# Performance work log

Measured on AMD Instinct MI355X. Metric: run time of the kernel, lower is better.

Reference implementation:

```python
import jax, jax.numpy as jnp
import numpy as np

N_NODES = 100000
N_EDGES = 1200000
NUM_GRAPHS = 128
IN_DIM = 5
HIDDEN = 64


def setup_inputs() -> dict:
    key = jax.random.key(0)
    ks = jax.random.split(key, 12)
    x = jax.random.normal(ks[0], (N_NODES, IN_DIM), dtype=jnp.float32)
    edge_index = jax.random.randint(ks[1], (2, N_EDGES), 0, N_NODES, dtype=jnp.int64 if jax.config.read('jax_enable_x64') else jnp.int32)
    batch = jnp.sort(jax.random.randint(ks[2], (N_NODES,), 0, NUM_GRAPHS, dtype=jnp.int32))
    s = lambda fan_in: 1.0 / np.sqrt(fan_in)
    return {
        'x': x,
        'edge_index': edge_index,
        'batch': batch,
        'w_rel1': jax.random.normal(ks[3], (IN_DIM, HIDDEN), dtype=jnp.float32) * s(IN_DIM),
        'b_rel1': jnp.zeros((HIDDEN,), dtype=jnp.float32),
        'w_root1': jax.random.normal(ks[4], (IN_DIM, HIDDEN), dtype=jnp.float32) * s(IN_DIM),
        'w_rel2': jax.random.normal(ks[5], (HIDDEN, HIDDEN), dtype=jnp.float32) * s(HIDDEN),
        'b_rel2': jnp.zeros((HIDDEN,), dtype=jnp.float32),
        'w_root2': jax.random.normal(ks[6], (HIDDEN, HIDDEN), dtype=jnp.float32) * s(HIDDEN),
        'w_h1': jax.random.normal(ks[7], (2 * HIDDEN, HIDDEN), dtype=jnp.float32) * s(2 * HIDDEN),
        'b_h1': jnp.zeros((HIDDEN,), dtype=jnp.float32),
        'w_h2': jax.random.normal(ks[8], (HIDDEN, 1), dtype=jnp.float32) * s(HIDDEN),
        'b_h2': jnp.zeros((1,), dtype=jnp.float32),
    }


def _graph_conv(x, src, dst, w_rel, b_rel, w_root):
    # PyG GraphConv (aggr='add'): out = aggr(x_src -> dst) @ W_rel + b_rel + x @ W_root
    agg = jax.ops.segment_sum(x[src], dst, num_segments=N_NODES)
    return agg @ w_rel + b_rel + x @ w_root


def reference(x, edge_index, batch,
              w_rel1, b_rel1, w_root1,
              w_rel2, b_rel2, w_root2,
              w_h1, b_h1, w_h2, b_h2):
    src, dst = edge_index[0], edge_index[1]
    h = jax.nn.relu(_graph_conv(x, src, dst, w_rel1, b_rel1, w_root1))
    h = jax.nn.relu(_graph_conv(h, src, dst, w_rel2, b_rel2, w_root2))
    # global add + mean pooling over graphs
    add_pool = jax.ops.segment_sum(h, batch, num_segments=NUM_GRAPHS)
    counts = jax.ops.segment_sum(jnp.ones((N_NODES,), h.dtype), batch, num_segments=NUM_GRAPHS)
    mean_pool = add_pool / jnp.maximum(counts, 1.0)[:, None]
    g = jnp.concatenate([mean_pool, add_pool], axis=1)  # [G, 2*HIDDEN]
    out = jax.nn.relu(g @ w_h1 + b_h1) @ w_h2 + b_h2
    return out.squeeze(-1)
```

## Files before the change

kernel.cpp:

```cpp
#include <hip/hip_runtime.h>
#include <hip/hip_bf16.h>

#define N_NODES    100000
#define N_EDGES    1200000
#define NUM_GRAPHS 128
#define IN_DIM     5
#define HIDDEN     64
#define M_TILES    (N_NODES / 16)
#define NI4        (N_EDGES / 4)

#define CB    391
#define CBLK  256
#define EPB   ((NI4 + CBLK - 1) / CBLK)

typedef __attribute__((ext_vector_type(8))) short short8;
typedef __attribute__((ext_vector_type(4))) float f32x4;

__device__ __forceinline__ unsigned short f2bs(float f) {
    union { float f; unsigned u; } v; v.f = f;
    return (unsigned short)((v.u + 0x7FFFu + ((v.u >> 16) & 1u)) >> 16);
}
__device__ __forceinline__ float bs2f(unsigned short s) {
    union { unsigned u; float f; } v; v.u = ((unsigned)s) << 16;
    return v.f;
}
__device__ __forceinline__ float blo(unsigned p) { return bs2f((unsigned short)(p & 0xffff)); }
__device__ __forceinline__ float bhi(unsigned p) { return bs2f((unsigned short)(p >> 16)); }
__device__ __forceinline__ unsigned pack2(float a, float b) {
    return ((unsigned)f2bs(b) << 16) | (unsigned)f2bs(a);
}

__device__ __forceinline__ unsigned char f2f8(float f) {
    union { float f; unsigned u; } v; v.f = f * 0x1p-120f;
    unsigned u = v.u + 0x7FFFFu + ((v.u >> 20) & 1u);
    return (unsigned char)(u >> 20);
}
__device__ __forceinline__ float f82f(unsigned b) {
    union { unsigned u; float f; } v; v.u = (b & 0x7Fu) << 20;
    return v.f * 0x1p120f;
}


__global__ void coarse_count(const int* __restrict__ dst, int* __restrict__ gcnt,
                             const float* __restrict__ x, uint4* __restrict__ xb) {
    __shared__ int h[CB];
    int t = threadIdx.x, b = blockIdx.x;
    for (int i = t; i < CB; i += 256) h[i] = 0;
    __syncthreads();
    int i0 = b * EPB, i1 = min(i0 + EPB, NI4);
    for (int i = i0 + t; i < i1; i += 256) {
        int4 d = ((const int4*)dst)[i];
        atomicAdd(&h[d.x >> 8], 1);
        atomicAdd(&h[d.y >> 8], 1);
        atomicAdd(&h[d.z >> 8], 1);
        atomicAdd(&h[d.w >> 8], 1);
    }
    __syncthreads();
    for (int i = t; i < CB; i += 256) gcnt[b * CB + i] = h[i];

    for (int n = b * 256 + t; n < N_NODES; n += CBLK * 256) {
        const float* xr = x + (size_t)n * IN_DIM;
        uint4 o;
        o.x = pack2(xr[0], xr[1]);
        o.y = pack2(xr[2], xr[3]);
        o.z = pack2(xr[4], 0.0f);
        o.w = 0u;
        xb[n] = o;
    }
}

__global__ void block_scan(int* __restrict__ gcnt, int* __restrict__ btot) {
    __shared__ int s[CBLK];
    int k = blockIdx.x, t = threadIdx.x;
    int v = gcnt[t * CB + k];
    s[t] = v;
    __syncthreads();
    for (int off = 1; off < CBLK; off <<= 1) {
        int u = (t >= off) ? s[t - off] : 0;
        __syncthreads();
        s[t] += u;
        __syncthreads();
    }
    gcnt[t * CB + k] = s[t] - v;
    if (t == CBLK - 1) btot[k] = s[t];
}

__global__ void bucket_scan(const int* __restrict__ btot, int* __restrict__ bstart,
                            float* __restrict__ add_pool, int* __restrict__ ptr) {
    __shared__ int s[512];
    int t = threadIdx.x;
    int v = (t < CB) ? btot[t] : 0;
    s[t] = v;
    __syncthreads();
    for (int off = 1; off < 512; off <<= 1) {
        int u = (t >= off) ? s[t - off] : 0;
        __syncthreads();
        s[t] += u;
        __syncthreads();
    }
    if (t < CB) bstart[t] = s[t] - v;
    if (t == 0) { bstart[CB] = N_EDGES; ptr[N_NODES] = N_EDGES; }
    for (int i = t; i < NUM_GRAPHS * HIDDEN; i += 512) add_pool[i] = 0.0f;
}

__global__ void partition_k(const int* __restrict__ src, const int* __restrict__ dst,
                            const int* __restrict__ gcnt, const int* __restrict__ bstart,
                            int* __restrict__ part) {
    __shared__ int base[CB];
    __shared__ int h[CB];
    int t = threadIdx.x, b = blockIdx.x;
    for (int i = t; i < CB; i += 256) {
        base[i] = bstart[i] + gcnt[b * CB + i];
        h[i] = 0;
    }
    __syncthreads();
    int i0 = b * EPB, i1 = min(i0 + EPB, NI4);
    for (int i = i0 + t; i < i1; i += 256) {
        int4 s4 = ((const int4*)src)[i];
        int4 d4 = ((const int4*)dst)[i];
        int k, r;
        k = d4.x >> 8; r = atomicAdd(&h[k], 1); part[base[k] + r] = s4.x | ((d4.x & 255) << 17);
        k = d4.y >> 8; r = atomicAdd(&h[k], 1); part[base[k] + r] = s4.y | ((d4.y & 255) << 17);
        k = d4.z >> 8; r = atomicAdd(&h[k], 1); part[base[k] + r] = s4.z | ((d4.z & 255) << 17);
        k = d4.w >> 8; r = atomicAdd(&h[k], 1); part[base[k] + r] = s4.w | ((d4.w & 255) << 17);
    }
}

__global__ void fine_gather1(const int* __restrict__ part, const int* __restrict__ bstart,
                             int* __restrict__ ptr, int* __restrict__ esrc,
                             const uint4* __restrict__ xb,
                             const float* __restrict__ x,
                             const float* __restrict__ w_rel1,
                             const float* __restrict__ b_rel1,
                             const float* __restrict__ w_root1,
                             unsigned short* __restrict__ h1,
                             unsigned char* __restrict__ h1f8) {
    __shared__ int fh[256];
    __shared__ int fo[256];
    __shared__ int fr[256];
    int k = blockIdx.x, t = threadIdx.x;
    int e0 = bstart[k], e1 = bstart[k + 1];
    fh[t] = 0; fr[t] = 0;
    __syncthreads();
    for (int e = e0 + t; e < e1; e += 256)
        atomicAdd(&fh[(part[e] >> 17) & 255], 1);
    __syncthreads();
    int v = fh[t];
    fo[t] = v;
    __syncthreads();
    for (int off = 1; off < 256; off <<= 1) {
        int u = (t >= off) ? fo[t - off] : 0;
        __syncthreads();
        fo[t] += u;
        __syncthreads();
    }
    int excl = fo[t] - v;
    int n_t = (k << 8) + t;
    if (n_t < N_NODES) ptr[n_t] = e0 + excl;
    fh[t] = excl;
    __syncthreads();
    for (int e = e0 + t; e < e1; e += 256) {
        int p = part[e];
        int d = (p >> 17) & 255;
        int r = atomicAdd(&fr[d], 1);
        esrc[e0 + fh[d] + r] = p & 0x1FFFF;
    }
    __syncthreads();

    int ql = t & 15;
    int g  = t >> 4;
    float wr[IN_DIM][4], wo[IN_DIM][4], bias[4];
#pragma unroll
    for (int j = 0; j < 4; ++j) {
        int ch = ql * 4 + j;
        bias[j] = b_rel1[ch];
#pragma unroll
        for (int kk = 0; kk < IN_DIM; ++kk) {
            wr[kk][j] = w_rel1[kk * HIDDEN + ch];
            wo[kk][j] = w_root1[kk * HIDDEN + ch];
        }
    }

    for (int nl = g; nl < 256; nl += 16) {
        int n = (k << 8) + nl;
        if (n >= N_NODES) break;
        int start = e0 + fh[nl];
        int end   = (nl < 255) ? (e0 + fh[nl + 1]) : e1;
        float a[IN_DIM] = {0.f, 0.f, 0.f, 0.f, 0.f};
        for (int e = start + ql; e < end; e += 16) {
            uint4 p = xb[esrc[e]];
            a[0] += blo(p.x); a[1] += bhi(p.x);
            a[2] += blo(p.y); a[3] += bhi(p.y);
            a[4] += blo(p.z);
        }
#pragma unroll
        for (int kk = 0; kk < IN_DIM; ++kk) {
            a[kk] += __shfl_xor(a[kk], 1, 64);
            a[kk] += __shfl_xor(a[kk], 2, 64);
            a[kk] += __shfl_xor(a[kk], 4, 64);
            a[kk] += __shfl_xor(a[kk], 8, 64);
        }
        float xr[IN_DIM];
#pragma unroll
        for (int kk = 0; kk < IN_DIM; ++kk) xr[kk] = x[(size_t)n * IN_DIM + kk];

        unsigned short hv[4];
        unsigned char  hf[4];
#pragma unroll
        for (int j = 0; j < 4; ++j) {
            float acc = bias[j];
#pragma unroll
            for (int kk = 0; kk < IN_DIM; ++kk)
                acc += a[kk] * wr[kk][j] + xr[kk] * wo[kk][j];
            float h = fmaxf(acc, 0.0f);
            hv[j] = f2bs(h);
            hf[j] = f2f8(h);
        }
        ushort4 v4; v4.x = hv[0]; v4.y = hv[1]; v4.z = hv[2]; v4.w = hv[3];
        *(ushort4*)(h1 + (size_t)n * HIDDEN + ql * 4) = v4;
        uchar4 c4; c4.x = hf[0]; c4.y = hf[1]; c4.z = hf[2]; c4.w = hf[3];
        *(uchar4*)(h1f8 + (size_t)n * HIDDEN + ql * 4) = c4;
    }
}


__global__ void gather2_fp8(const unsigned* __restrict__ rows,
                            const int* __restrict__ ptr,
                            const int* __restrict__ esrc,
                            uint2* __restrict__ agg2) {
    int t    = threadIdx.x;
    int ql   = t & 15;
    int grp  = (blockIdx.x * blockDim.x + t) >> 4;
    int ngrp = (gridDim.x * blockDim.x) >> 4;

    for (int n = grp; n < N_NODES; n += ngrp) {
        int start = ptr[n], end = ptr[n + 1];
        float4 a0 = {0.f,0.f,0.f,0.f}, a1 = a0, a2 = a0, a3 = a0;
        int e = start;
        for (; e + 3 < end; e += 4) {
            int s0 = esrc[e], s1 = esrc[e + 1], s2 = esrc[e + 2], s3 = esrc[e + 3];
            unsigned r0 = rows[(size_t)s0 * 16 + ql];
            unsigned r1 = rows[(size_t)s1 * 16 + ql];
            unsigned r2 = rows[(size_t)s2 * 16 + ql];
            unsigned r3 = rows[(size_t)s3 * 16 + ql];
            a0.x += f82f(r0); a0.y += f82f(r0 >> 8); a0.z += f82f(r0 >> 16); a0.w += f82f(r0 >> 24);
            a1.x += f82f(r1); a1.y += f82f(r1 >> 8); a1.z += f82f(r1 >> 16); a1.w += f82f(r1 >> 24);
            a2.x += f82f(r2); a2.y += f82f(r2 >> 8); a2.z += f82f(r2 >> 16); a2.w += f82f(r2 >> 24);
            a3.x += f82f(r3); a3.y += f82f(r3 >> 8); a3.z += f82f(r3 >> 16); a3.w += f82f(r3 >> 24);
        }
        for (; e < end; ++e) {
            unsigned r0 = rows[(size_t)esrc[e] * 16 + ql];
            a0.x += f82f(r0); a0.y += f82f(r0 >> 8); a0.z += f82f(r0 >> 16); a0.w += f82f(r0 >> 24);
        }
        float4 a;
        a.x = (a0.x + a1.x) + (a2.x + a3.x);
        a.y = (a0.y + a1.y) + (a2.y + a3.y);
        a.z = (a0.z + a1.z) + (a2.z + a3.z);
        a.w = (a0.w + a1.w) + (a2.w + a3.w);
        uint2 o;
        o.x = pack2(a.x, a.y);
        o.y = pack2(a.z, a.w);
        agg2[(size_t)n * 16 + ql] = o;
    }
}

__global__ void mlp2_pool(const unsigned short* __restrict__ agg2,
                          const unsigned short* __restrict__ h1,
                          const float* __restrict__ w_rel2,
                          const float* __restrict__ b_rel2,
                          const float* __restrict__ w_root2,
                          const int* __restrict__ batch,
                          float* __restrict__ add_pool) {
    int lane = threadIdx.x & 63;
    int wv   = threadIdx.x >> 6;
    int row  = lane & 15;
    int quad = lane >> 4;
    int n    = wv * 16 + row;

    short8 bwr[2], bwo[2];
#pragma unroll
    for (int s = 0; s < 2; ++s)
#pragma unroll
        for (int j = 0; j < 8; ++j) {
            int k = 32 * s + quad * 8 + j;
            bwr[s][j] = (short)f2bs(w_rel2[k * HIDDEN + n]);
            bwo[s][j] = (short)f2bs(w_root2[k * HIDDEN + n]);
        }
    float bias = b_rel2[n];

    for (int t = blockIdx.x; t < M_TILES; t += gridDim.x) {
        int m0 = t * 16;
        size_t rbase = (size_t)(m0 + row) * HIDDEN;
        short8 aa0 = *(const short8*)(agg2 + rbase + quad * 8);
        short8 aa1 = *(const short8*)(agg2 + rbase + 32 + quad * 8);
        short8 ah0 = *(const short8*)(h1   + rbase + quad * 8);
        short8 ah1 = *(const short8*)(h1   + rbase + 32 + quad * 8);

        f32x4 acc = {bias, bias, bias, bias};
        acc = __builtin_amdgcn_mfma_f32_16x16x32_bf16(aa0, bwr[0], acc, 0, 0, 0);
        acc = __builtin_amdgcn_mfma_f32_16x16x32_bf16(aa1, bwr[1], acc, 0, 0, 0);
        acc = __builtin_amdgcn_mfma_f32_16x16x32_bf16(ah0, bwo[0], acc, 0, 0, 0);
        acc = __builtin_amdgcn_mfma_f32_16x16x32_bf16(ah1, bwo[1], acc, 0, 0, 0);

        float hv0 = fmaxf(acc[0], 0.0f), hv1 = fmaxf(acc[1], 0.0f);
        float hv2 = fmaxf(acc[2], 0.0f), hv3 = fmaxf(acc[3], 0.0f);

        int gLo = batch[m0], gHi = batch[m0 + 15];
        if (gLo == gHi) {
            float s = (hv0 + hv1) + (hv2 + hv3);
            s += __shfl_xor(s, 16, 64);
            s += __shfl_xor(s, 32, 64);
            if (quad == 0)
                atomicAdd(&add_pool[gLo * HIDDEN + n], s);
        } else {
            int m = m0 + quad * 4;
            atomicAdd(&add_pool[batch[m]     * HIDDEN + n], hv0);
            atomicAdd(&add_pool[batch[m + 1] * HIDDEN + n], hv1);
            atomicAdd(&add_pool[batch[m + 2] * HIDDEN + n], hv2);
            atomicAdd(&add_pool[batch[m + 3] * HIDDEN + n], hv3);
        }
    }
}

__device__ __forceinline__ int lower_bound_i(const int* a, int n, int v) {
    int lo = 0, hi = n;
    while (lo < hi) { int mid = (lo + hi) >> 1; if (a[mid] < v) lo = mid + 1; else hi = mid; }
    return lo;
}

__global__ void head_mlp(const float* __restrict__ add_pool,
                         const int* __restrict__ batch,
                         const float* __restrict__ w_h1,
                         const float* __restrict__ b_h1,
                         const float* __restrict__ w_h2,
                         const float* __restrict__ b_h2,
                         float* __restrict__ out) {
    int g = blockIdx.x, t = threadIdx.x;

    __shared__ int s_cnt;
    if (t == 0) {
        int start = lower_bound_i(batch, N_NODES, g);
        int end   = lower_bound_i(batch, N_NODES, g + 1);
        s_cnt = end - start;
    }
    __syncthreads();
    float cnt = fmaxf((float)s_cnt, 1.0f);

    __shared__ float sg[2 * HIDDEN];
    float add = add_pool[(size_t)g * HIDDEN + t];
    sg[t]          = add / cnt;
    sg[HIDDEN + t] = add;
    __syncthreads();

    float hid = b_h1[t];
#pragma unroll 16
    for (int i = 0; i < 2 * HIDDEN; ++i)
        hid += sg[i] * w_h1[i * HIDDEN + t];
    hid = fmaxf(hid, 0.0f);

    float res = hid * w_h2[t];
    for (int off = 32; off > 0; off >>= 1)
        res += __shfl_down(res, off, 64);
    if (t == 0) out[g] = res + b_h2[0];
}

extern "C" void kernel_launch(void* const* d_in, const int* in_sizes, int n_in,
                              void* d_out, int out_size, void* d_ws, size_t ws_size,
                              hipStream_t stream) {
    const float* x       = (const float*)d_in[0];
    const int*   ei      = (const int*)d_in[1];
    const int*   src     = ei;
    const int*   dst     = ei + N_EDGES;
    const int*   batch   = (const int*)d_in[2];
    const float* w_rel1  = (const float*)d_in[3];
    const float* b_rel1  = (const float*)d_in[4];
    const float* w_root1 = (const float*)d_in[5];
    const float* w_rel2  = (const float*)d_in[6];
    const float* b_rel2  = (const float*)d_in[7];
    const float* w_root2 = (const float*)d_in[8];
    const float* w_h1    = (const float*)d_in[9];
    const float* b_h1    = (const float*)d_in[10];
    const float* w_h2    = (const float*)d_in[11];
    const float* b_h2    = (const float*)d_in[12];
    float* out = (float*)d_out;

    int* base = (int*)d_ws;
    int*   gcnt     = base;
    int*   btot     = gcnt + ((CBLK * CB + 3) & ~3);
    int*   bstart   = btot + ((CB + 3) & ~3);
    float* add_pool = (float*)(bstart + ((CB + 1 + 3) & ~3));
    int*   ptr      = (int*)(add_pool + NUM_GRAPHS * HIDDEN);
    int*   part     = ptr + ((N_NODES + 1 + 3) & ~3);
    int*   esrc     = part + N_EDGES;
    unsigned short* h1   = (unsigned short*)(esrc + N_EDGES);
    unsigned short* agg2 = h1 + (size_t)N_NODES * HIDDEN;
    unsigned char*  h1f8 = (unsigned char*)(agg2 + (size_t)N_NODES * HIDDEN);
    uint4*          xb   = (uint4*)(h1f8 + (size_t)N_NODES * HIDDEN);

    coarse_count<<<CBLK, 256, 0, stream>>>(dst, gcnt, x, xb);
    block_scan<<<CB, CBLK, 0, stream>>>(gcnt, btot);
    bucket_scan<<<1, 512, 0, stream>>>(btot, bstart, add_pool, ptr);
    partition_k<<<CBLK, 256, 0, stream>>>(src, dst, gcnt, bstart, part);

    fine_gather1<<<CB, 256, 0, stream>>>(part, bstart, ptr, esrc, xb, x,
                                         w_rel1, b_rel1, w_root1, h1, h1f8);
    gather2_fp8<<<2048, 256, 0, stream>>>((const unsigned*)h1f8, ptr, esrc, (uint2*)agg2);
    mlp2_pool<<<2048, 256, 0, stream>>>(agg2, h1, w_rel2, b_rel2, w_root2, batch, add_pool);
    head_mlp<<<NUM_GRAPHS, 64, 0, stream>>>(add_pool, batch, w_h1, b_h1, w_h2, b_h2, out);
}
```

Before: 195.4 us.

## Fuse CSR build kernels into one cooperative launch and use hardware fp8 conversion

The four preprocessing kernels (coarse count, per-bucket scan, bucket scan, partition) are merged into a single cooperative kernel that uses grid-wide syncs between phases. This removes three kernel launch gaps and their inter-kernel drain. The old four-launch path stays as a fallback if the cooperative launch fails. Separately, the fp8 gather decode now uses the packed hardware fp8-to-f32 conversion builtin when it is available, replacing manual bit manipulation. That conversion assumes the hardware fp8 format matches the custom encoding produced by f2f8, which looks like an E4M3-style bias trick and may not match exactly.

```diff
diff --git a/kernel.cpp b/kernel.cpp
--- a/kernel.cpp
+++ b/kernel.cpp
@@ -1,5 +1,8 @@
 #include <hip/hip_runtime.h>
 #include <hip/hip_bf16.h>
+#include <hip/hip_cooperative_groups.h>
+
+namespace cg = cooperative_groups;
 
 #define N_NODES    100000
 #define N_EDGES    1200000
@@ -15,6 +18,13 @@
 
 typedef __attribute__((ext_vector_type(8))) short short8;
 typedef __attribute__((ext_vector_type(4))) float f32x4;
+typedef __attribute__((ext_vector_type(2))) float f32x2;
+
+#if defined(__has_builtin)
+#if __has_builtin(__builtin_amdgcn_cvt_pk_f32_fp8)
+#define HAS_HWF8 1
+#endif
+#endif
 
 __device__ __forceinline__ unsigned short f2bs(float f) {
     union { float f; unsigned u; } v; v.f = f;
@@ -40,11 +50,28 @@
     return v.f * 0x1p120f;
 }
 
-
-__global__ void coarse_count(const int* __restrict__ dst, int* __restrict__ gcnt,
-                             const float* __restrict__ x, uint4* __restrict__ xb) {
+__device__ __forceinline__ void acc8(float4& a, unsigned r) {
+#ifdef HAS_HWF8
+    f32x2 lo = __builtin_amdgcn_cvt_pk_f32_fp8((int)r, false);
+    f32x2 hi = __builtin_amdgcn_cvt_pk_f32_fp8((int)r, true);
+    a.x += lo[0]; a.y += lo[1]; a.z += hi[0]; a.w += hi[1];
+#else
+    a.x += f82f(r); a.y += f82f(r >> 8); a.z += f82f(r >> 16); a.w += f82f(r >> 24);
+#endif
+}
+
+
+__global__ void coop_build(const int* __restrict__ src, const int* __restrict__ dst,
+                           int* __restrict__ gcnt, int* __restrict__ btot,
+                           int* __restrict__ bstart, int* __restrict__ part,
+                           int* __restrict__ ptr, float* __restrict__ add_pool,
+                           const float* __restrict__ x, uint4* __restrict__ xb) {
+    cg::grid_group grid = cg::this_grid();
     __shared__ int h[CB];
+    __shared__ int base[CB];
+    __shared__ int s[CBLK];
     int t = threadIdx.x, b = blockIdx.x;
+
     for (int i = t; i < CB; i += 256) h[i] = 0;
     __syncthreads();
     int i0 = b * EPB, i1 = min(i0 + EPB, NI4);
@@ -57,7 +84,98 @@
     }
     __syncthreads();
     for (int i = t; i < CB; i += 256) gcnt[b * CB + i] = h[i];
-
+    for (int n = b * 256 + t; n < N_NODES; n += CBLK * 256) {
+        const float* xr = x + (size_t)n * IN_DIM;
+        uint4 o;
+        o.x = pack2(xr[0], xr[1]);
+        o.y = pack2(xr[2], xr[3]);
+        o.z = pack2(xr[4], 0.0f);
+        o.w = 0u;
+        xb[n] = o;
+    }
+    __threadfence();
+    grid.sync();
+
+    for (int k = b; k < CB; k += CBLK) {
+        int v = gcnt[t * CB + k];
+        s[t] = v;
+        __syncthreads();
+        for (int off = 1; off < CBLK; off <<= 1) {
+            int u = (t >= off) ? s[t - off] : 0;
+            __syncthreads();
+            s[t] += u;
+            __syncthreads();
+        }
+        gcnt[t * CB + k] = s[t] - v;
+        if (t == CBLK - 1) btot[k] = s[t];
+        __syncthreads();
+    }
+    __threadfence();
+    grid.sync();
+
+    if (b == 0) {
+        if (t < 64) {
+            int cbase = t * 7;
+            int loc[7];
+            int sum = 0;
+#pragma unroll
+            for (int j = 0; j < 7; ++j) {
+                int idx = cbase + j;
+                int c = (idx < CB) ? btot[idx] : 0;
+                loc[j] = sum; sum += c;
+            }
+            int inc = sum;
+#pragma unroll
+            for (int off = 1; off < 64; off <<= 1) {
+                int u = __shfl_up(inc, off, 64);
+                if (t >= off) inc += u;
+            }
+            int excl = inc - sum;
+#pragma unroll
+            for (int j = 0; j < 7; ++j) {
+                int idx = cbase + j;
+                if (idx < CB) bstart[idx] = excl + loc[j];
+            }
+        }
+        if (t == 0) { bstart[CB] = N_EDGES; ptr[N_NODES] = N_EDGES; }
+    } else if (b == 1) {
+        for (int i = t; i < NUM_GRAPHS * HIDDEN; i += 256) add_pool[i] = 0.0f;
+    }
+    __threadfence();
+    grid.sync();
+
+    for (int i = t; i < CB; i += 256) {
+        base[i] = bstart[i] + gcnt[b * CB + i];
+        h[i] = 0;
+    }
+    __syncthreads();
+    for (int i = i0 + t; i < i1; i += 256) {
+        int4 s4 = ((const int4*)src)[i];
+        int4 d4 = ((const int4*)dst)[i];
+        int k, r;
+        k = d4.x >> 8; r = atomicAdd(&h[k], 1); part[base[k] + r] = s4.x | ((d4.x & 255) << 17);
+        k = d4.y >> 8; r = atomicAdd(&h[k], 1); part[base[k] + r] = s4.y | ((d4.y & 255) << 17);
+        k = d4.z >> 8; r = atomicAdd(&h[k], 1); part[base[k] + r] = s4.z | ((d4.z & 255) << 17);
+        k = d4.w >> 8; r = atomicAdd(&h[k], 1); part[base[k] + r] = s4.w | ((d4.w & 255) << 17);
+    }
+}
+
+__global__ void coarse_count(const int* __restrict__ dst, int* __restrict__ gcnt,
+                             const float* __restrict__ x, uint4* __restrict__ xb) {
+    __shared__ int h[CB];
+    int t = threadIdx.x, b = blockIdx.x;
+    for (int i = t; i < CB; i += 256) h[i] = 0;
+    __syncthreads();
+    int i0 = b * EPB, i1 = min(i0 + EPB, NI4);
+    for (int i = i0 + t; i < i1; i += 256) {
+        int4 d = ((const int4*)dst)[i];
+        atomicAdd(&h[d.x >> 8], 1);
+        atomicAdd(&h[d.y >> 8], 1);
+        atomicAdd(&h[d.z >> 8], 1);
+        atomicAdd(&h[d.w >> 8], 1);
+    }
+    __syncthreads();
+    for (int i = t; i < CB; i += 256) gcnt[b * CB + i] = h[i];
     for (int n = b * 256 + t; n < N_NODES; n += CBLK * 256) {
         const float* xr = x + (size_t)n * IN_DIM;
         uint4 o;
@@ -243,14 +361,11 @@
             unsigned r1 = rows[(size_t)s1 * 16 + ql];
             unsigned r2 = rows[(size_t)s2 * 16 + ql];
             unsigned r3 = rows[(size_t)s3 * 16 + ql];
-            a0.x += f82f(r0); a0.y += f82f(r0 >> 8); a0.z += f82f(r0 >> 16); a0.w += f82f(r0 >> 24);
-            a1.x += f82f(r1); a1.y += f82f(r1 >> 8); a1.z += f82f(r1 >> 16); a1.w += f82f(r1 >> 24);
-            a2.x += f82f(r2); a2.y += f82f(r2 >> 8); a2.z += f82f(r2 >> 16); a2.w += f82f(r2 >> 24);
-            a3.x += f82f(r3); a3.y += f82f(r3 >> 8); a3.z += f82f(r3 >> 16); a3.w += f82f(r3 >> 24);
+            acc8(a0, r0); acc8(a1, r1); acc8(a2, r2); acc8(a3, r3);
         }
         for (; e < end; ++e) {
             unsigned r0 = rows[(size_t)esrc[e] * 16 + ql];
-            a0.x += f82f(r0); a0.y += f82f(r0 >> 8); a0.z += f82f(r0 >> 16); a0.w += f82f(r0 >> 24);
+            acc8(a0, r0);
         }
         float4 a;
         a.x = (a0.x + a1.x) + (a2.x + a3.x);
@@ -397,10 +512,19 @@
     unsigned char*  h1f8 = (unsigned char*)(agg2 + (size_t)N_NODES * HIDDEN);
     uint4*          xb   = (uint4*)(h1f8 + (size_t)N_NODES * HIDDEN);
 
-    coarse_count<<<CBLK, 256, 0, stream>>>(dst, gcnt, x, xb);
-    block_scan<<<CB, CBLK, 0, stream>>>(gcnt, btot);
-    bucket_scan<<<1, 512, 0, stream>>>(btot, bstart, add_pool, ptr);
-    partition_k<<<CBLK, 256, 0, stream>>>(src, dst, gcnt, bstart, part);
+    {
+        void* ka[] = { (void*)&src, (void*)&dst, (void*)&gcnt, (void*)&btot,
+                       (void*)&bstart, (void*)&part, (void*)&ptr, (void*)&add_pool,
+                       (void*)&x, (void*)&xb };
+        hipError_t err = hipLaunchCooperativeKernel((const void*)coop_build,
+                                                    dim3(CBLK), dim3(256), ka, 0, stream);
+        if (err != hipSuccess) {
+            coarse_count<<<CBLK, 256, 0, stream>>>(dst, gcnt, x, xb);
+            block_scan<<<CB, CBLK, 0, stream>>>(gcnt, btot);
+            bucket_scan<<<1, 512, 0, stream>>>(btot, bstart, add_pool, ptr);
+            partition_k<<<CBLK, 256, 0, stream>>>(src, dst, gcnt, bstart, part);
+        }
+    }
 
     fine_gather1<<<CB, 256, 0, stream>>>(part, bstart, ptr, esrc, xb, x,
                                          w_rel1, b_rel1, w_root1, h1, h1f8);
```

Result: slower. 370.8 us (+89.8%).

## Fold scan kernels into partition, halve bucket width, use hardware fp8 convert

Applied to the files above, without the earlier changes.

The separate block_scan and bucket_scan launches are removed. Each partition_k block now computes its own prefix and the bucket totals by reading the whole gcnt column, followed by a wave-level scan, and add_pool zeroing moves into coarse_count. Buckets shrink from 256 to 128 nodes (782 buckets), which doubles fine_gather1 blocks and reduces per-block imbalance. The fp8 decode in gather2 uses the hardware packed conversion builtin when available. The cost is redundant per-block reads of gcnt (256×782 ints per block) and half-idle threads in the fine scan.

```diff
diff --git a/kernel.cpp b/kernel.cpp
--- a/kernel.cpp
+++ b/kernel.cpp
@@ -9,12 +9,19 @@
 #define M_TILES    (N_NODES / 16)
 #define NI4        (N_EDGES / 4)
 
-#define CB    391
+#define CB    782
 #define CBLK  256
 #define EPB   ((NI4 + CBLK - 1) / CBLK)
 
 typedef __attribute__((ext_vector_type(8))) short short8;
 typedef __attribute__((ext_vector_type(4))) float f32x4;
+typedef __attribute__((ext_vector_type(2))) float f32x2;
+
+#if defined(__has_builtin)
+#if __has_builtin(__builtin_amdgcn_cvt_pk_f32_fp8)
+#define HAS_HWF8 1
+#endif
+#endif
 
 __device__ __forceinline__ unsigned short f2bs(float f) {
     union { float f; unsigned u; } v; v.f = f;
@@ -40,9 +47,20 @@
     return v.f * 0x1p120f;
 }
 
+__device__ __forceinline__ void acc8(float4& a, unsigned r) {
+#ifdef HAS_HWF8
+    f32x2 lo = __builtin_amdgcn_cvt_pk_f32_fp8((int)r, false);
+    f32x2 hi = __builtin_amdgcn_cvt_pk_f32_fp8((int)r, true);
+    a.x += lo[0]; a.y += lo[1]; a.z += hi[0]; a.w += hi[1];
+#else
+    a.x += f82f(r); a.y += f82f(r >> 8); a.z += f82f(r >> 16); a.w += f82f(r >> 24);
+#endif
+}
+
 
 __global__ void coarse_count(const int* __restrict__ dst, int* __restrict__ gcnt,
-                             const float* __restrict__ x, uint4* __restrict__ xb) {
+                             const float* __restrict__ x, uint4* __restrict__ xb,
+                             float* __restrict__ add_pool, int* __restrict__ ptr) {
     __shared__ int h[CB];
     int t = threadIdx.x, b = blockIdx.x;
     for (int i = t; i < CB; i += 256) h[i] = 0;
@@ -50,10 +68,10 @@
     int i0 = b * EPB, i1 = min(i0 + EPB, NI4);
     for (int i = i0 + t; i < i1; i += 256) {
         int4 d = ((const int4*)dst)[i];
-        atomicAdd(&h[d.x >> 8], 1);
-        atomicAdd(&h[d.y >> 8], 1);
-        atomicAdd(&h[d.z >> 8], 1);
-        atomicAdd(&h[d.w >> 8], 1);
+        atomicAdd(&h[d.x >> 7], 1);
+        atomicAdd(&h[d.y >> 7], 1);
+        atomicAdd(&h[d.z >> 7], 1);
+        atomicAdd(&h[d.w >> 7], 1);
     }
     __syncthreads();
     for (int i = t; i < CB; i += 256) gcnt[b * CB + i] = h[i];
@@ -67,62 +85,75 @@
         o.w = 0u;
         xb[n] = o;
     }
-}
-
-__global__ void block_scan(int* __restrict__ gcnt, int* __restrict__ btot) {
-    __shared__ int s[CBLK];
-    int k = blockIdx.x, t = threadIdx.x;
-    int v = gcnt[t * CB + k];
-    s[t] = v;
-    __syncthreads();
-    for (int off = 1; off < CBLK; off <<= 1) {
-        int u = (t >= off) ? s[t - off] : 0;
-        __syncthreads();
-        s[t] += u;
-        __syncthreads();
-    }
-    gcnt[t * CB + k] = s[t] - v;
-    if (t == CBLK - 1) btot[k] = s[t];
-}
-
-__global__ void bucket_scan(const int* __restrict__ btot, int* __restrict__ bstart,
-                            float* __restrict__ add_pool, int* __restrict__ ptr) {
-    __shared__ int s[512];
-    int t = threadIdx.x;
-    int v = (t < CB) ? btot[t] : 0;
-    s[t] = v;
-    __syncthreads();
-    for (int off = 1; off < 512; off <<= 1) {
-        int u = (t >= off) ? s[t - off] : 0;
-        __syncthreads();
-        s[t] += u;
-        __syncthreads();
-    }
-    if (t < CB) bstart[t] = s[t] - v;
-    if (t == 0) { bstart[CB] = N_EDGES; ptr[N_NODES] = N_EDGES; }
-    for (int i = t; i < NUM_GRAPHS * HIDDEN; i += 512) add_pool[i] = 0.0f;
+    if (b == 0) {
+        for (int i = t; i < NUM_GRAPHS * HIDDEN; i += 256) add_pool[i] = 0.0f;
+        if (t == 0) ptr[N_NODES] = N_EDGES;
+    }
 }
 
 __global__ void partition_k(const int* __restrict__ src, const int* __restrict__ dst,
-                            const int* __restrict__ gcnt, const int* __restrict__ bstart,
+                            const int* __restrict__ gcnt, int* __restrict__ bstart,
                             int* __restrict__ part) {
-    __shared__ int base[CB];
+    __shared__ int sp[CB];
+    __shared__ int st[CB];
     __shared__ int h[CB];
     int t = threadIdx.x, b = blockIdx.x;
-    for (int i = t; i < CB; i += 256) {
-        base[i] = bstart[i] + gcnt[b * CB + i];
-        h[i] = 0;
-    }
-    __syncthreads();
+
+    for (int k = t; k < CB; k += 256) {
+        int pref = 0, tot = 0;
+        for (int bp = 0; bp < CBLK; ++bp) {
+            int v = gcnt[bp * CB + k];
+            tot += v;
+            if (bp < b) pref += v;
+        }
+        sp[k] = pref;
+        st[k] = tot;
+        h[k] = 0;
+    }
+    __syncthreads();
+
+    if (t < 64) {
+        int loc[13];
+        int base_i = t * 13;
+        int sum = 0;
+#pragma unroll
+        for (int j = 0; j < 13; ++j) {
+            int idx = base_i + j;
+            int c = (idx < CB) ? st[idx] : 0;
+            loc[j] = sum; sum += c;
+        }
+        int inc = sum;
+#pragma unroll
+        for (int off = 1; off < 64; off <<= 1) {
+            int u = __shfl_up(inc, off, 64);
+            if (t >= off) inc += u;
+        }
+        int excl = inc - sum;
+#pragma unroll
+        for (int j = 0; j < 13; ++j) {
+            int idx = base_i + j;
+            if (idx < CB) st[idx] = excl + loc[j];
+        }
+    }
+    __syncthreads();
+
+    for (int k = t; k < CB; k += 256) {
+        int bs = st[k];
+        sp[k] = bs + sp[k];
+        if (b == 0) bstart[k] = bs;
+    }
+    if (b == 0 && t == 0) bstart[CB] = N_EDGES;
+    __syncthreads();
+
     int i0 = b * EPB, i1 = min(i0 + EPB, NI4);
     for (int i = i0 + t; i < i1; i += 256) {
         int4 s4 = ((const int4*)src)[i];
         int4 d4 = ((const int4*)dst)[i];
         int k, r;
-        k = d4.x >> 8; r = atomicAdd(&h[k], 1); part[base[k] + r] = s4.x | ((d4.x & 255) << 17);
-        k = d4.y >> 8; r = atomicAdd(&h[k], 1); part[base[k] + r] = s4.y | ((d4.y & 255) << 17);
-        k = d4.z >> 8; r = atomicAdd(&h[k], 1); part[base[k] + r] = s4.z | ((d4.z & 255) << 17);
-        k = d4.w >> 8; r = atomicAdd(&h[k], 1); part[base[k] + r] = s4.w | ((d4.w & 255) << 17);
+        k = d4.x >> 7; r = atomicAdd(&h[k], 1); part[sp[k] + r] = s4.x | ((d4.x & 127) << 17);
+        k = d4.y >> 7; r = atomicAdd(&h[k], 1); part[sp[k] + r] = s4.y | ((d4.y & 127) << 17);
+        k = d4.z >> 7; r = atomicAdd(&h[k], 1); part[sp[k] + r] = s4.z | ((d4.z & 127) << 17);
+        k = d4.w >> 7; r = atomicAdd(&h[k], 1); part[sp[k] + r] = s4.w | ((d4.w & 127) << 17);
     }
 }
 
@@ -135,33 +166,35 @@
                              const float* __restrict__ w_root1,
                              unsigned short* __restrict__ h1,
                              unsigned char* __restrict__ h1f8) {
-    __shared__ int fh[256];
-    __shared__ int fo[256];
-    __shared__ int fr[256];
+    __shared__ int fh[128];
+    __shared__ int fo[128];
+    __shared__ int fr[128];
     int k = blockIdx.x, t = threadIdx.x;
     int e0 = bstart[k], e1 = bstart[k + 1];
-    fh[t] = 0; fr[t] = 0;
+    if (t < 128) { fh[t] = 0; fr[t] = 0; }
     __syncthreads();
     for (int e = e0 + t; e < e1; e += 256)
-        atomicAdd(&fh[(part[e] >> 17) & 255], 1);
-    __syncthreads();
-    int v = fh[t];
-    fo[t] = v;
-    __syncthreads();
-    for (int off = 1; off < 256; off <<= 1) {
-        int u = (t >= off) ? fo[t - off] : 0;
+        atomicAdd(&fh[(part[e] >> 17) & 127], 1);
+    __syncthreads();
+    int v = (t < 128) ? fh[t] : 0;
+    if (t < 128) fo[t] = v;
+    __syncthreads();
+    for (int off = 1; off < 128; off <<= 1) {
+        int u = (t >= off && t < 128) ? fo[t - off] : 0;
         __syncthreads();
-        fo[t] += u;
+        if (t < 128) fo[t] += u;
         __syncthreads();
     }
-    int excl = fo[t] - v;
-    int n_t = (k << 8) + t;
-    if (n_t < N_NODES) ptr[n_t] = e0 + excl;
-    fh[t] = excl;
+    if (t < 128) {
+        int excl = fo[t] - v;
+        int n_t = (k << 7) + t;
+        if (n_t < N_NODES) ptr[n_t] = e0 + excl;
+        fh[t] = excl;
+    }
     __syncthreads();
     for (int e = e0 + t; e < e1; e += 256) {
         int p = part[e];
-        int d = (p >> 17) & 255;
+        int d = (p >> 17) & 127;
         int r = atomicAdd(&fr[d], 1);
         esrc[e0 + fh[d] + r] = p & 0x1FFFF;
     }
@@ -181,11 +214,11 @@
         }
     }
 
-    for (int nl = g; nl < 256; nl += 16) {
-        int n = (k << 8) + nl;
+    for (int nl = g; nl < 128; nl += 16) {
+        int n = (k << 7) + nl;
         if (n >= N_NODES) break;
         int start = e0 + fh[nl];
-        int end   = (nl < 255) ? (e0 + fh[nl + 1]) : e1;
+        int end   = (nl < 127) ? (e0 + fh[nl + 1]) : e1;
         float a[IN_DIM] = {0.f, 0.f, 0.f, 0.f, 0.f};
         for (int e = start + ql; e < end; e += 16) {
             uint4 p = xb[esrc[e]];
@@ -243,14 +276,11 @@
             unsigned r1 = rows[(size_t)s1 * 16 + ql];
             unsigned r2 = rows[(size_t)s2 * 16 + ql];
             unsigned r3 = rows[(size_t)s3 * 16 + ql];
-            a0.x += f82f(r0); a0.y += f82f(r0 >> 8); a0.z += f82f(r0 >> 16); a0.w += f82f(r0 >> 24);
-            a1.x += f82f(r1); a1.y += f82f(r1 >> 8); a1.z += f82f(r1 >> 16); a1.w += f82f(r1 >> 24);
-            a2.x += f82f(r2); a2.y += f82f(r2 >> 8); a2.z += f82f(r2 >> 16); a2.w += f82f(r2 >> 24);
-            a3.x += f82f(r3); a3.y += f82f(r3 >> 8); a3.z += f82f(r3 >> 16); a3.w += f82f(r3 >> 24);
+            acc8(a0, r0); acc8(a1, r1); acc8(a2, r2); acc8(a3, r3);
         }
         for (; e < end; ++e) {
             unsigned r0 = rows[(size_t)esrc[e] * 16 + ql];
-            a0.x += f82f(r0); a0.y += f82f(r0 >> 8); a0.z += f82f(r0 >> 16); a0.w += f82f(r0 >> 24);
+            acc8(a0, r0);
         }
         float4 a;
         a.x = (a0.x + a1.x) + (a2.x + a3.x);
@@ -386,8 +416,7 @@
 
     int* base = (int*)d_ws;
     int*   gcnt     = base;
-    int*   btot     = gcnt + ((CBLK * CB + 3) & ~3);
-    int*   bstart   = btot + ((CB + 3) & ~3);
+    int*   bstart   = gcnt + ((CBLK * CB + 3) & ~3);
     float* add_pool = (float*)(bstart + ((CB + 1 + 3) & ~3));
     int*   ptr      = (int*)(add_pool + NUM_GRAPHS * HIDDEN);
     int*   part     = ptr + ((N_NODES + 1 + 3) & ~3);
@@ -397,9 +426,7 @@
     unsigned char*  h1f8 = (unsigned char*)(agg2 + (size_t)N_NODES * HIDDEN);
     uint4*          xb   = (uint4*)(h1f8 + (size_t)N_NODES * HIDDEN);
 
-    coarse_count<<<CBLK, 256, 0, stream>>>(dst, gcnt, x, xb);
-    block_scan<<<CB, CBLK, 0, stream>>>(gcnt, btot);
-    bucket_scan<<<1, 512, 0, stream>>>(btot, bstart, add_pool, ptr);
+    coarse_count<<<CBLK, 256, 0, stream>>>(dst, gcnt, x, xb, add_pool, ptr);
     partition_k<<<CBLK, 256, 0, stream>>>(src, dst, gcnt, bstart, part);
 
     fine_gather1<<<CB, 256, 0, stream>>>(part, bstart, ptr, esrc, xb, x,
```

Measured after the change: 227.9 us. 1.17x slower.
